# Kernel tuning notes

Measured on AMD Instinct MI355X. Metric: run time of the kernel, lower is better.

The kernel has to match this reference:

```python
import jax, jax.numpy as jnp
import numpy as np

N_HEAD = 16
D_HEAD = 64
HIDDEN = 1024
T = 2048
B = 4


def setup_inputs() -> dict:
    key = jax.random.key(0)
    k1, k2, k3, k4, k5 = jax.random.split(key, 5)
    qkv_out = (2 * N_HEAD + 1) * D_HEAD  # 2112
    return {
        "x": jax.random.normal(k1, (B, T, HIDDEN), dtype=jnp.float32),
        "w_qkv": jax.random.normal(k2, (qkv_out, HIDDEN), dtype=jnp.float32) * (HIDDEN ** -0.5),
        "b_qkv": jax.random.normal(k3, (qkv_out,), dtype=jnp.float32) * 0.02,
        "w_out": jax.random.normal(k4, (HIDDEN, D_HEAD), dtype=jnp.float32) * (D_HEAD ** -0.5),
        "b_out": jax.random.normal(k5, (HIDDEN,), dtype=jnp.float32) * 0.02,
    }


def reference(x, w_qkv, b_qkv, w_out, b_out):
    bs, t, h = x.shape
    scale = D_HEAD ** -0.5
    qkv = x @ w_qkv.T + b_qkv  # [b, t, (2H+1)*dh]
    q, k, v = jnp.split(qkv, [N_HEAD * D_HEAD, 2 * N_HEAD * D_HEAD], axis=-1)
    q = q.reshape(bs, t, N_HEAD, D_HEAD)
    k = k.reshape(bs, t, N_HEAD, D_HEAD)
    v = v.reshape(bs, t, D_HEAD)  # single V head shared across all heads
    # attn_score: [b, h, i, j]
    attn_score = jnp.einsum("bihd,bjhd->bhij", q, k) * scale
    # causal mask: -inf above diagonal
    causal = jnp.triu(jnp.full((t, t), -jnp.inf, dtype=attn_score.dtype), 1)
    attn_score = attn_score + causal
    attn_prob = jax.nn.softmax(attn_score, axis=-1)  # dropout is identity in eval
    # shared V across heads: [b,h,i,j] x [b,j,d] -> [b,h,i,d]
    attn_vec = jnp.einsum("bhij,bjd->bhid", attn_prob, v)
    m_attn_vec = jnp.mean(attn_vec, axis=1)  # mean over heads -> [b, t, d_head]
    out = m_attn_vec @ w_out.T + b_out  # [b, t, hidden]
    return out, attn_vec
```

## Files before the change

### kernel.cpp

```cpp
#include <hip/hip_runtime.h>
#include <hip/hip_bf16.h>
#include <math.h>

#define NHEAD 16
#define DHEAD 64
#define HIDDEN 1024
#define TSEQ 2048
#define BATCH 4
#define QKV_OUT 2112
#define BT (BATCH * TSEQ)

typedef __attribute__((ext_vector_type(8))) short bf16x8;
typedef __attribute__((ext_vector_type(4))) float floatx4;

static __device__ __forceinline__ short f2bf(float x) {
  __hip_bfloat16 h = __float2bfloat16(x);
  return *reinterpret_cast<short*>(&h);
}

#define MFMA16(a, b, c) __builtin_amdgcn_mfma_f32_16x16x32_bf16(a, b, c, 0, 0, 0)

__global__ __launch_bounds__(256) void f32_to_bf16(
    const float* __restrict__ src, short* __restrict__ dst, int n) {
  const int i = (blockIdx.x * 256 + threadIdx.x) * 8;
  if (i >= n) return;
  float4 a = *(const float4*)&src[i];
  float4 b = *(const float4*)&src[i + 4];
  short o[8];
  o[0] = f2bf(a.x); o[1] = f2bf(a.y); o[2] = f2bf(a.z); o[3] = f2bf(a.w);
  o[4] = f2bf(b.x); o[5] = f2bf(b.y); o[6] = f2bf(b.z); o[7] = f2bf(b.w);
  *(uint4*)&dst[i] = *(uint4*)o;
}

#define QK_BM 128
#define QK_BN 64
#define QK_BK 64

template <typename OUT_T>
__global__ __launch_bounds__(256) void gemm_mfma_bf16(
    const short* __restrict__ A, const short* __restrict__ B,
    const float* __restrict__ bias, OUT_T* __restrict__ C,
    int M, int N, int K) {
  __shared__ short As[QK_BM][72];
  __shared__ short Bs[QK_BN][72];

  const int tid = threadIdx.x;
  const int lane = tid & 63;
  const int wv = tid >> 6;
  const int ln = lane & 15;
  const int grp = lane >> 4;
  const int wm = wv >> 1;
  const int wn = wv & 1;
  const int rowbase = blockIdx.y * QK_BM;
  const int colbase = blockIdx.x * QK_BN;

  const int ar = tid >> 1, ac = (tid & 1) * 32;
  const int br = tid >> 2, bc = (tid & 3) * 16;

  floatx4 acc[4][2];
#pragma unroll
  for (int m = 0; m < 4; ++m)
#pragma unroll
    for (int n = 0; n < 2; ++n) acc[m][n] = (floatx4){0.f, 0.f, 0.f, 0.f};

  const short* ap = A + (size_t)(rowbase + ar) * K + ac;
  const short* bp = B + (size_t)(colbase + br) * K + bc;

  uint4 a0 = *(const uint4*)(ap + 0);
  uint4 a1 = *(const uint4*)(ap + 8);
  uint4 a2 = *(const uint4*)(ap + 16);
  uint4 a3 = *(const uint4*)(ap + 24);
  uint4 b0 = *(const uint4*)(bp + 0);
  uint4 b1 = *(const uint4*)(bp + 8);

  for (int k0 = 0; k0 < K; k0 += QK_BK) {
    __syncthreads();
    *(uint4*)&As[ar][ac + 0] = a0;
    *(uint4*)&As[ar][ac + 8] = a1;
    *(uint4*)&As[ar][ac + 16] = a2;
    *(uint4*)&As[ar][ac + 24] = a3;
    *(uint4*)&Bs[br][bc + 0] = b0;
    *(uint4*)&Bs[br][bc + 8] = b1;
    __syncthreads();

    if (k0 + QK_BK < K) {
      ap += QK_BK;
      bp += QK_BK;
      a0 = *(const uint4*)(ap + 0);
      a1 = *(const uint4*)(ap + 8);
      a2 = *(const uint4*)(ap + 16);
      a3 = *(const uint4*)(ap + 24);
      b0 = *(const uint4*)(bp + 0);
      b1 = *(const uint4*)(bp + 8);
    }

#pragma unroll
    for (int ks = 0; ks < 2; ++ks) {
      bf16x8 bfrag[2];
#pragma unroll
      for (int n = 0; n < 2; ++n)
        bfrag[n] = *(const bf16x8*)&Bs[wn * 32 + n * 16 + ln][ks * 32 + grp * 8];
#pragma unroll
      for (int m = 0; m < 4; ++m) {
        bf16x8 af = *(const bf16x8*)&As[wm * 64 + m * 16 + ln][ks * 32 + grp * 8];
#pragma unroll
        for (int n = 0; n < 2; ++n)
          acc[m][n] = MFMA16(af, bfrag[n], acc[m][n]);
      }
    }
  }

#pragma unroll
  for (int n = 0; n < 2; ++n) {
    const int col = colbase + wn * 32 + n * 16 + ln;
    const float bv = bias[col];
#pragma unroll
    for (int m = 0; m < 4; ++m) {
#pragma unroll
      for (int r = 0; r < 4; ++r) {
        const int row = rowbase + wm * 64 + m * 16 + grp * 4 + r;
        const float v = acc[m][n][r] + bv;
        if constexpr (sizeof(OUT_T) == 2)
          C[(size_t)row * N + col] = f2bf(v);
        else
          C[(size_t)row * N + col] = v;
      }
    }
  }
}

__global__ __launch_bounds__(256) void transpose_v(
    const short* __restrict__ qkv, short* __restrict__ vt) {
  __shared__ short tile[64][72];
  const int tt = blockIdx.x;
  const int b = blockIdx.y;
  const int tid = threadIdx.x;
  const int li = tid >> 2;
  const int lc = (tid & 3) * 16;

  const short* src = qkv + (size_t)(b * TSEQ + tt * 64 + li) * QKV_OUT + 2048 + lc;
  *(uint4*)&tile[li][lc] = *(const uint4*)src;
  *(uint4*)&tile[li][lc + 8] = *(const uint4*)(src + 8);
  __syncthreads();
  short tmp[16];
#pragma unroll
  for (int u = 0; u < 16; ++u) tmp[u] = tile[lc + u][li];
  short* dst = vt + (size_t)(b * 64 + li) * TSEQ + tt * 64 + lc;
  *(uint4*)dst = *(uint4*)&tmp[0];
  *(uint4*)(dst + 8) = *(uint4*)&tmp[8];
}

#define CH 8

__global__ __launch_bounds__(256) void attn_partial(
    const short* __restrict__ qkv, const short* __restrict__ vt,
    float* __restrict__ attn_vec, float* __restrict__ pO,
    float* __restrict__ pL) {
  __shared__ short Ks[64][72];
  __shared__ short Vt[64][72];
  __shared__ short Ps[64][72];

  const int x = gridDim.x - 1 - blockIdx.x;
  int it, jc;
  if (x < 8) {
    it = x; jc = 0;
  } else if (x < 24) {
    it = 8 + ((x - 8) >> 1); jc = (x - 8) & 1;
  } else if (x < 48) {
    it = 16 + (x - 24) / 3; jc = (x - 24) % 3;
  } else {
    it = 24 + ((x - 48) >> 2); jc = (x - 48) & 3;
  }
  const int jstart = jc * CH;
  const int jend = min(jstart + CH, it + 1);

  const int tid = threadIdx.x;
  const int h = blockIdx.y;
  const int b = blockIdx.z;
  const int lane = tid & 63;
  const int wv = tid >> 6;
  const int ln = lane & 15;
  const int grp = lane >> 4;
  const int qbase = wv * 16;
  const int sli = tid & 63;
  const int slc = (tid >> 6) * 16;
  const float CEXP = 0.18033688f;

  const short* qptr = qkv + (size_t)(b * TSEQ + it * 64 + qbase + ln) * QKV_OUT + h * 64;
  const bf16x8 bq0 = *(const bf16x8*)(qptr + grp * 8);
  const bf16x8 bq1 = *(const bf16x8*)(qptr + 32 + grp * 8);

  floatx4 oT[4];
#pragma unroll
  for (int m = 0; m < 4; ++m) oT[m] = (floatx4){0.f, 0.f, 0.f, 0.f};
  float lsum = 0.f;

  const short* ks0 = qkv + (size_t)(b * TSEQ + jstart * 64 + sli) * QKV_OUT + 1024 + h * 64 + slc;
  const short* vs0 = vt + (size_t)(b * 64 + sli) * TSEQ + jstart * 64 + slc;
  uint4 kr0 = *(const uint4*)ks0;
  uint4 kr1 = *(const uint4*)(ks0 + 8);
  uint4 vr0 = *(const uint4*)vs0;
  uint4 vr1 = *(const uint4*)(vs0 + 8);

  for (int jt = jstart; jt < jend; ++jt) {
    __syncthreads();
    *(uint4*)&Ks[sli][slc] = kr0;
    *(uint4*)&Ks[sli][slc + 8] = kr1;
    *(uint4*)&Vt[sli][slc] = vr0;
    *(uint4*)&Vt[sli][slc + 8] = vr1;
    __syncthreads();

    if (jt + 1 < jend) {
      const short* kn =
          qkv + (size_t)(b * TSEQ + (jt + 1) * 64 + sli) * QKV_OUT + 1024 + h * 64 + slc;
      const short* vn = vt + (size_t)(b * 64 + sli) * TSEQ + (jt + 1) * 64 + slc;
      kr0 = *(const uint4*)kn;
      kr1 = *(const uint4*)(kn + 8);
      vr0 = *(const uint4*)vn;
      vr1 = *(const uint4*)(vn + 8);
    }

    floatx4 st[4];
    __builtin_amdgcn_s_setprio(1);
#pragma unroll
    for (int m = 0; m < 4; ++m) {
      bf16x8 ak0 = *(const bf16x8*)&Ks[m * 16 + ln][grp * 8];
      bf16x8 ak1 = *(const bf16x8*)&Ks[m * 16 + ln][32 + grp * 8];
      floatx4 a = (floatx4){0.f, 0.f, 0.f, 0.f};
      a = MFMA16(ak0, bq0, a);
      a = MFMA16(ak1, bq1, a);
      st[m] = a;
    }
    __builtin_amdgcn_s_setprio(0);

    if (jt == it) {
#pragma unroll
      for (int m = 0; m < 4; ++m)
#pragma unroll
        for (int r = 0; r < 4; ++r)
          if (m * 16 + grp * 4 + r > qbase + ln) st[m][r] = -INFINITY;
    }

#pragma unroll
    for (int m = 0; m < 4; ++m) {
      float p0 = exp2f(CEXP * st[m][0]);
      float p1 = exp2f(CEXP * st[m][1]);
      float p2 = exp2f(CEXP * st[m][2]);
      float p3 = exp2f(CEXP * st[m][3]);
      lsum += (p0 + p1) + (p2 + p3);
      short pk[4] = {f2bf(p0), f2bf(p1), f2bf(p2), f2bf(p3)};
      *(uint2*)&Ps[qbase + ln][m * 16 + grp * 4] = *(uint2*)pk;
    }

    bf16x8 bp0 = *(const bf16x8*)&Ps[qbase + ln][grp * 8];
    bf16x8 bp1 = *(const bf16x8*)&Ps[qbase + ln][32 + grp * 8];
    __builtin_amdgcn_s_setprio(1);
#pragma unroll
    for (int m = 0; m < 4; ++m) {
      bf16x8 av0 = *(const bf16x8*)&Vt[m * 16 + ln][grp * 8];
      bf16x8 av1 = *(const bf16x8*)&Vt[m * 16 + ln][32 + grp * 8];
      oT[m] = MFMA16(av0, bp0, oT[m]);
      oT[m] = MFMA16(av1, bp1, oT[m]);
    }
    __builtin_amdgcn_s_setprio(0);
  }

  lsum += __shfl_xor(lsum, 16);
  lsum += __shfl_xor(lsum, 32);

  if (it < 8) {
    const float inv = 1.f / lsum;
    float* orow =
        attn_vec + ((size_t)(b * NHEAD + h) * TSEQ + it * 64 + qbase + ln) * DHEAD;
#pragma unroll
    for (int m = 0; m < 4; ++m) {
      float4 o4;
      o4.x = oT[m][0] * inv;
      o4.y = oT[m][1] * inv;
      o4.z = oT[m][2] * inv;
      o4.w = oT[m][3] * inv;
      *(float4*)&orow[m * 16 + grp * 4] = o4;
    }
  } else {
    const int slot = (it < 16) ? (it - 8) * 2 + jc
                   : (it < 24) ? 16 + (it - 16) * 3 + jc
                               : 40 + (it - 24) * 4 + jc;
    const size_t sbase = (size_t)(b * NHEAD + h) * 72 + slot;
    float* prow = pO + sbase * 4096 + (size_t)(qbase + ln) * 64;
#pragma unroll
    for (int m = 0; m < 4; ++m) {
      float4 o4;
      o4.x = oT[m][0]; o4.y = oT[m][1]; o4.z = oT[m][2]; o4.w = oT[m][3];
      *(float4*)&prow[m * 16 + grp * 4] = o4;
    }
    if (grp == 0) pL[sbase * 64 + qbase + ln] = lsum;
  }
}

__global__ __launch_bounds__(256) void attn_combine(
    const float* __restrict__ pO, const float* __restrict__ pL,
    float* __restrict__ attn_vec) {
  const int it = 8 + blockIdx.x;
  const int h = blockIdx.y;
  const int b = blockIdx.z;
  const int nch = (it < 16) ? 2 : (it < 24) ? 3 : 4;
  const int slot0 = (it < 16) ? (it - 8) * 2
                  : (it < 24) ? 16 + (it - 16) * 3
                              : 40 + (it - 24) * 4;
  const int q = threadIdx.x >> 2;
  const int dbase = (threadIdx.x & 3) * 16;
  const size_t base = (size_t)(b * NHEAD + h) * 72 + slot0;

  float4 acc[4];
#pragma unroll
  for (int u = 0; u < 4; ++u) acc[u] = (float4){0.f, 0.f, 0.f, 0.f};
  float l = 0.f;
  for (int c = 0; c < nch; ++c) {
    const float* pr = pO + (base + c) * 4096 + (size_t)q * 64 + dbase;
#pragma unroll
    for (int u = 0; u < 4; ++u) {
      float4 v = *(const float4*)&pr[u * 4];
      acc[u].x += v.x; acc[u].y += v.y; acc[u].z += v.z; acc[u].w += v.w;
    }
    l += pL[(base + c) * 64 + q];
  }
  const float inv = 1.f / l;
  float* orow =
      attn_vec + ((size_t)(b * NHEAD + h) * TSEQ + it * 64 + q) * DHEAD + dbase;
#pragma unroll
  for (int u = 0; u < 4; ++u) {
    float4 o4;
    o4.x = acc[u].x * inv; o4.y = acc[u].y * inv;
    o4.z = acc[u].z * inv; o4.w = acc[u].w * inv;
    *(float4*)&orow[u * 4] = o4;
  }
}

__global__ __launch_bounds__(256) void mean_heads(
    const float* __restrict__ attn_vec, short* __restrict__ m) {
  const int gid = blockIdx.x * 256 + threadIdx.x;
  const int d2 = (gid & 31) * 2;
  const int t = (gid >> 5) & (TSEQ - 1);
  const int b = gid >> 16;
  float s0 = 0.f, s1 = 0.f;
#pragma unroll
  for (int h = 0; h < NHEAD; ++h) {
    const float* p = &attn_vec[(((size_t)(b * NHEAD + h) * TSEQ) + t) * DHEAD + d2];
    s0 += p[0];
    s1 += p[1];
  }
  short pk[2] = {f2bf(s0 * (1.f / 16.f)), f2bf(s1 * (1.f / 16.f))};
  *(uint*)&m[gid * 2] = *(uint*)pk;
}

extern "C" void kernel_launch(void* const* d_in, const int* in_sizes, int n_in,
                              void* d_out, int out_size, void* d_ws, size_t ws_size,
                              hipStream_t stream) {
  const float* x     = (const float*)d_in[0];
  const float* w_qkv = (const float*)d_in[1];
  const float* b_qkv = (const float*)d_in[2];
  const float* w_out = (const float*)d_in[3];
  const float* b_out = (const float*)d_in[4];

  float* out      = (float*)d_out;
  float* attn_vec = out + (size_t)BT * HIDDEN;

  short* qkv_bf  = (short*)d_ws;
  short* vt_bf   = qkv_bf + (size_t)BT * QKV_OUT;
  short* wout_bf = vt_bf + (size_t)BATCH * DHEAD * TSEQ;
  short* m_attn  = wout_bf + (size_t)HIDDEN * DHEAD;
  char*  xbase   = (char*)(m_attn + (size_t)BT * DHEAD);
  short* x_bf    = (short*)xbase;
  short* w_bf    = x_bf + (size_t)BT * HIDDEN;
  float* pO      = (float*)xbase;
  float* pL      = pO + (size_t)64 * 72 * 4096;

  f32_to_bf16<<<dim3(BT * HIDDEN / 8 / 256), 256, 0, stream>>>(
      x, x_bf, BT * HIDDEN);
  f32_to_bf16<<<dim3(QKV_OUT * HIDDEN / 8 / 256), 256, 0, stream>>>(
      w_qkv, w_bf, QKV_OUT * HIDDEN);
  f32_to_bf16<<<dim3(HIDDEN * DHEAD / 8 / 256), 256, 0, stream>>>(
      w_out, wout_bf, HIDDEN * DHEAD);

  gemm_mfma_bf16<short><<<dim3(QKV_OUT / QK_BN, BT / QK_BM), 256, 0, stream>>>(
      x_bf, w_bf, b_qkv, qkv_bf, BT, QKV_OUT, HIDDEN);

  transpose_v<<<dim3(TSEQ / 64, BATCH), 256, 0, stream>>>(qkv_bf, vt_bf);

  attn_partial<<<dim3(80, NHEAD, BATCH), 256, 0, stream>>>(
      qkv_bf, vt_bf, attn_vec, pO, pL);

  attn_combine<<<dim3(24, NHEAD, BATCH), 256, 0, stream>>>(pO, pL, attn_vec);

  mean_heads<<<dim3(BT * DHEAD / 2 / 256), 256, 0, stream>>>(attn_vec, m_attn);

  gemm_mfma_bf16<float><<<dim3(HIDDEN / QK_BN, BT / QK_BM), 256, 0, stream>>>(
      m_attn, wout_bf, b_out, out, BT, HIDDEN, DHEAD);
}
```

Baseline: 286.4 us.

## Widen attention query tile to 128 rows with 512-thread blocks and two-way KV split

The attention kernel now processes 128 query rows per block with 8 waves instead of 64 rows with 4 waves, so each loaded K/V tile is reused by twice as many queries. The KV range is split into at most two chunks of 16 tiles, which simplifies the partial-slot indexing and the combine kernel. Waves whose rows lie entirely above the causal boundary skip the compute. The trade-off is fewer, larger blocks (1536 versus 5120), longer per-block serial loops, and less even load balance across the causal triangle.

```diff
diff --git a/kernel.cpp b/kernel.cpp
--- a/kernel.cpp
+++ b/kernel.cpp
@@ -150,29 +150,25 @@
   *(uint4*)(dst + 8) = *(uint4*)&tmp[8];
 }
 
-#define CH 8
-
-__global__ __launch_bounds__(256) void attn_partial(
+#define QB 128
+
+__global__ __launch_bounds__(512) void attn_partial(
     const short* __restrict__ qkv, const short* __restrict__ vt,
     float* __restrict__ attn_vec, float* __restrict__ pO,
     float* __restrict__ pL) {
   __shared__ short Ks[64][72];
   __shared__ short Vt[64][72];
-  __shared__ short Ps[64][72];
-
-  const int x = gridDim.x - 1 - blockIdx.x;
+  __shared__ short Ps[128][72];
+
+  const int x = (int)gridDim.x - 1 - (int)blockIdx.x;
   int it, jc;
   if (x < 8) {
     it = x; jc = 0;
-  } else if (x < 24) {
+  } else {
     it = 8 + ((x - 8) >> 1); jc = (x - 8) & 1;
-  } else if (x < 48) {
-    it = 16 + (x - 24) / 3; jc = (x - 24) % 3;
-  } else {
-    it = 24 + ((x - 48) >> 2); jc = (x - 48) & 3;
-  }
-  const int jstart = jc * CH;
-  const int jend = min(jstart + CH, it + 1);
+  }
+  const int jstart = jc * 16;
+  const int jend = min(jstart + 16, 2 * it + 2);
 
   const int tid = threadIdx.x;
   const int h = blockIdx.y;
@@ -182,11 +178,12 @@
   const int ln = lane & 15;
   const int grp = lane >> 4;
   const int qbase = wv * 16;
-  const int sli = tid & 63;
-  const int slc = (tid >> 6) * 16;
+  const int sr = tid >> 3;
+  const int sc = (tid & 7) * 8;
   const float CEXP = 0.18033688f;
 
-  const short* qptr = qkv + (size_t)(b * TSEQ + it * 64 + qbase + ln) * QKV_OUT + h * 64;
+  const short* qptr =
+      qkv + (size_t)(b * TSEQ + it * QB + qbase + ln) * QKV_OUT + h * 64;
   const bf16x8 bq0 = *(const bf16x8*)(qptr + grp * 8);
   const bf16x8 bq1 = *(const bf16x8*)(qptr + 32 + grp * 8);
 
@@ -195,74 +192,73 @@
   for (int m = 0; m < 4; ++m) oT[m] = (floatx4){0.f, 0.f, 0.f, 0.f};
   float lsum = 0.f;
 
-  const short* ks0 = qkv + (size_t)(b * TSEQ + jstart * 64 + sli) * QKV_OUT + 1024 + h * 64 + slc;
-  const short* vs0 = vt + (size_t)(b * 64 + sli) * TSEQ + jstart * 64 + slc;
-  uint4 kr0 = *(const uint4*)ks0;
-  uint4 kr1 = *(const uint4*)(ks0 + 8);
-  uint4 vr0 = *(const uint4*)vs0;
-  uint4 vr1 = *(const uint4*)(vs0 + 8);
+  const short* ks0 =
+      qkv + (size_t)(b * TSEQ + jstart * 64 + sr) * QKV_OUT + 1024 + h * 64 + sc;
+  const short* vs0 = vt + (size_t)(b * 64 + sr) * TSEQ + jstart * 64 + sc;
+  uint4 kr = *(const uint4*)ks0;
+  uint4 vr = *(const uint4*)vs0;
 
   for (int jt = jstart; jt < jend; ++jt) {
     __syncthreads();
-    *(uint4*)&Ks[sli][slc] = kr0;
-    *(uint4*)&Ks[sli][slc + 8] = kr1;
-    *(uint4*)&Vt[sli][slc] = vr0;
-    *(uint4*)&Vt[sli][slc + 8] = vr1;
+    *(uint4*)&Ks[sr][sc] = kr;
+    *(uint4*)&Vt[sr][sc] = vr;
     __syncthreads();
 
     if (jt + 1 < jend) {
       const short* kn =
-          qkv + (size_t)(b * TSEQ + (jt + 1) * 64 + sli) * QKV_OUT + 1024 + h * 64 + slc;
-      const short* vn = vt + (size_t)(b * 64 + sli) * TSEQ + (jt + 1) * 64 + slc;
-      kr0 = *(const uint4*)kn;
-      kr1 = *(const uint4*)(kn + 8);
-      vr0 = *(const uint4*)vn;
-      vr1 = *(const uint4*)(vn + 8);
-    }
-
-    floatx4 st[4];
-    __builtin_amdgcn_s_setprio(1);
-#pragma unroll
-    for (int m = 0; m < 4; ++m) {
-      bf16x8 ak0 = *(const bf16x8*)&Ks[m * 16 + ln][grp * 8];
-      bf16x8 ak1 = *(const bf16x8*)&Ks[m * 16 + ln][32 + grp * 8];
-      floatx4 a = (floatx4){0.f, 0.f, 0.f, 0.f};
-      a = MFMA16(ak0, bq0, a);
-      a = MFMA16(ak1, bq1, a);
-      st[m] = a;
-    }
-    __builtin_amdgcn_s_setprio(0);
-
-    if (jt == it) {
-#pragma unroll
-      for (int m = 0; m < 4; ++m)
-#pragma unroll
-        for (int r = 0; r < 4; ++r)
-          if (m * 16 + grp * 4 + r > qbase + ln) st[m][r] = -INFINITY;
-    }
-
-#pragma unroll
-    for (int m = 0; m < 4; ++m) {
-      float p0 = exp2f(CEXP * st[m][0]);
-      float p1 = exp2f(CEXP * st[m][1]);
-      float p2 = exp2f(CEXP * st[m][2]);
-      float p3 = exp2f(CEXP * st[m][3]);
-      lsum += (p0 + p1) + (p2 + p3);
-      short pk[4] = {f2bf(p0), f2bf(p1), f2bf(p2), f2bf(p3)};
-      *(uint2*)&Ps[qbase + ln][m * 16 + grp * 4] = *(uint2*)pk;
-    }
-
-    bf16x8 bp0 = *(const bf16x8*)&Ps[qbase + ln][grp * 8];
-    bf16x8 bp1 = *(const bf16x8*)&Ps[qbase + ln][32 + grp * 8];
-    __builtin_amdgcn_s_setprio(1);
-#pragma unroll
-    for (int m = 0; m < 4; ++m) {
-      bf16x8 av0 = *(const bf16x8*)&Vt[m * 16 + ln][grp * 8];
-      bf16x8 av1 = *(const bf16x8*)&Vt[m * 16 + ln][32 + grp * 8];
-      oT[m] = MFMA16(av0, bp0, oT[m]);
-      oT[m] = MFMA16(av1, bp1, oT[m]);
-    }
-    __builtin_amdgcn_s_setprio(0);
+          qkv + (size_t)(b * TSEQ + (jt + 1) * 64 + sr) * QKV_OUT + 1024 + h * 64 + sc;
+      const short* vn = vt + (size_t)(b * 64 + sr) * TSEQ + (jt + 1) * 64 + sc;
+      kr = *(const uint4*)kn;
+      vr = *(const uint4*)vn;
+    }
+
+    const int qg = it * QB + qbase;
+    if (qg + 15 >= jt * 64) {
+      floatx4 st[4];
+      __builtin_amdgcn_s_setprio(1);
+#pragma unroll
+      for (int m = 0; m < 4; ++m) {
+        bf16x8 ak0 = *(const bf16x8*)&Ks[m * 16 + ln][grp * 8];
+        bf16x8 ak1 = *(const bf16x8*)&Ks[m * 16 + ln][32 + grp * 8];
+        floatx4 a = (floatx4){0.f, 0.f, 0.f, 0.f};
+        a = MFMA16(ak0, bq0, a);
+        a = MFMA16(ak1, bq1, a);
+        st[m] = a;
+      }
+      __builtin_amdgcn_s_setprio(0);
+
+      const int dj = qg + ln - jt * 64;
+      if (dj < 63) {
+#pragma unroll
+        for (int m = 0; m < 4; ++m)
+#pragma unroll
+          for (int r = 0; r < 4; ++r)
+            if (m * 16 + grp * 4 + r > dj) st[m][r] = -INFINITY;
+      }
+
+#pragma unroll
+      for (int m = 0; m < 4; ++m) {
+        float p0 = exp2f(CEXP * st[m][0]);
+        float p1 = exp2f(CEXP * st[m][1]);
+        float p2 = exp2f(CEXP * st[m][2]);
+        float p3 = exp2f(CEXP * st[m][3]);
+        lsum += (p0 + p1) + (p2 + p3);
+        short pk[4] = {f2bf(p0), f2bf(p1), f2bf(p2), f2bf(p3)};
+        *(uint2*)&Ps[qbase + ln][m * 16 + grp * 4] = *(uint2*)pk;
+      }
+
+      bf16x8 bp0 = *(const bf16x8*)&Ps[qbase + ln][grp * 8];
+      bf16x8 bp1 = *(const bf16x8*)&Ps[qbase + ln][32 + grp * 8];
+      __builtin_amdgcn_s_setprio(1);
+#pragma unroll
+      for (int m = 0; m < 4; ++m) {
+        bf16x8 av0 = *(const bf16x8*)&Vt[m * 16 + ln][grp * 8];
+        bf16x8 av1 = *(const bf16x8*)&Vt[m * 16 + ln][32 + grp * 8];
+        oT[m] = MFMA16(av0, bp0, oT[m]);
+        oT[m] = MFMA16(av1, bp1, oT[m]);
+      }
+      __builtin_amdgcn_s_setprio(0);
+    }
   }
 
   lsum += __shfl_xor(lsum, 16);
@@ -271,7 +267,7 @@
   if (it < 8) {
     const float inv = 1.f / lsum;
     float* orow =
-        attn_vec + ((size_t)(b * NHEAD + h) * TSEQ + it * 64 + qbase + ln) * DHEAD;
+        attn_vec + ((size_t)(b * NHEAD + h) * TSEQ + it * QB + qbase + ln) * DHEAD;
 #pragma unroll
     for (int m = 0; m < 4; ++m) {
       float4 o4;
@@ -282,18 +278,16 @@
       *(float4*)&orow[m * 16 + grp * 4] = o4;
     }
   } else {
-    const int slot = (it < 16) ? (it - 8) * 2 + jc
-                   : (it < 24) ? 16 + (it - 16) * 3 + jc
-                               : 40 + (it - 24) * 4 + jc;
-    const size_t sbase = (size_t)(b * NHEAD + h) * 72 + slot;
-    float* prow = pO + sbase * 4096 + (size_t)(qbase + ln) * 64;
+    const int slot = (it - 8) * 2 + jc;
+    const size_t sbase = (size_t)(b * NHEAD + h) * 16 + slot;
+    float* prow = pO + sbase * 8192 + (size_t)(qbase + ln) * 64;
 #pragma unroll
     for (int m = 0; m < 4; ++m) {
       float4 o4;
       o4.x = oT[m][0]; o4.y = oT[m][1]; o4.z = oT[m][2]; o4.w = oT[m][3];
       *(float4*)&prow[m * 16 + grp * 4] = o4;
     }
-    if (grp == 0) pL[sbase * 64 + qbase + ln] = lsum;
+    if (grp == 0) pL[sbase * 128 + qbase + ln] = lsum;
   }
 }
 
@@ -303,32 +297,29 @@
   const int it = 8 + blockIdx.x;
   const int h = blockIdx.y;
   const int b = blockIdx.z;
-  const int nch = (it < 16) ? 2 : (it < 24) ? 3 : 4;
-  const int slot0 = (it < 16) ? (it - 8) * 2
-                  : (it < 24) ? 16 + (it - 16) * 3
-                              : 40 + (it - 24) * 4;
-  const int q = threadIdx.x >> 2;
-  const int dbase = (threadIdx.x & 3) * 16;
-  const size_t base = (size_t)(b * NHEAD + h) * 72 + slot0;
-
-  float4 acc[4];
-#pragma unroll
-  for (int u = 0; u < 4; ++u) acc[u] = (float4){0.f, 0.f, 0.f, 0.f};
+  const int q = threadIdx.x >> 1;
+  const int dbase = (threadIdx.x & 1) * 32;
+  const size_t base = (size_t)(b * NHEAD + h) * 16 + (it - 8) * 2;
+
+  float4 acc[8];
+#pragma unroll
+  for (int u = 0; u < 8; ++u) acc[u] = (float4){0.f, 0.f, 0.f, 0.f};
   float l = 0.f;
-  for (int c = 0; c < nch; ++c) {
-    const float* pr = pO + (base + c) * 4096 + (size_t)q * 64 + dbase;
-#pragma unroll
-    for (int u = 0; u < 4; ++u) {
+#pragma unroll
+  for (int c = 0; c < 2; ++c) {
+    const float* pr = pO + (base + c) * 8192 + (size_t)q * 64 + dbase;
+#pragma unroll
+    for (int u = 0; u < 8; ++u) {
       float4 v = *(const float4*)&pr[u * 4];
       acc[u].x += v.x; acc[u].y += v.y; acc[u].z += v.z; acc[u].w += v.w;
     }
-    l += pL[(base + c) * 64 + q];
+    l += pL[(base + c) * 128 + q];
   }
   const float inv = 1.f / l;
   float* orow =
-      attn_vec + ((size_t)(b * NHEAD + h) * TSEQ + it * 64 + q) * DHEAD + dbase;
-#pragma unroll
-  for (int u = 0; u < 4; ++u) {
+      attn_vec + ((size_t)(b * NHEAD + h) * TSEQ + it * QB + q) * DHEAD + dbase;
+#pragma unroll
+  for (int u = 0; u < 8; ++u) {
     float4 o4;
     o4.x = acc[u].x * inv; o4.y = acc[u].y * inv;
     o4.z = acc[u].z * inv; o4.w = acc[u].w * inv;
@@ -373,7 +364,7 @@
   short* x_bf    = (short*)xbase;
   short* w_bf    = x_bf + (size_t)BT * HIDDEN;
   float* pO      = (float*)xbase;
-  float* pL      = pO + (size_t)64 * 72 * 4096;
+  float* pL      = pO + (size_t)64 * 16 * 8192;
 
   f32_to_bf16<<<dim3(BT * HIDDEN / 8 / 256), 256, 0, stream>>>(
       x, x_bf, BT * HIDDEN);
@@ -387,10 +378,10 @@
 
   transpose_v<<<dim3(TSEQ / 64, BATCH), 256, 0, stream>>>(qkv_bf, vt_bf);
 
-  attn_partial<<<dim3(80, NHEAD, BATCH), 256, 0, stream>>>(
+  attn_partial<<<dim3(24, NHEAD, BATCH), 512, 0, stream>>>(
       qkv_bf, vt_bf, attn_vec, pO, pL);
 
-  attn_combine<<<dim3(24, NHEAD, BATCH), 256, 0, stream>>>(pO, pL, attn_vec);
+  attn_combine<<<dim3(8, NHEAD, BATCH), 256, 0, stream>>>(pO, pL, attn_vec);
 
   mean_heads<<<dim3(BT * DHEAD / 2 / 256), 256, 0, stream>>>(attn_vec, m_attn);
 
```

Result: no change. 285.5 us (-0.3%).
